# Kernel tuning notes

Hardware: AMD Instinct MI355X
Metric: run time of the kernel (lower is better)

## Reference

```python
import jax, jax.numpy as jnp
import numpy as np


def _gcn_norm(edge_index, n_nodes):
    # add self-loops, compute symmetric normalization coeffs (PyG gcn_norm)
    loop = jnp.arange(n_nodes, dtype=edge_index.dtype)
    src = jnp.concatenate([edge_index[0], loop])
    dst = jnp.concatenate([edge_index[1], loop])
    ones = jnp.ones(src.shape[0], dtype=jnp.float32)
    deg = jax.ops.segment_sum(ones, dst, num_segments=n_nodes)
    dinv = jnp.where(deg > 0, jax.lax.rsqrt(deg), 0.0)
    norm = dinv[src] * dinv[dst]  # (E + n_nodes,)
    return src, dst, norm


def _gcn_conv(x, W, b, src, dst, norm, n_nodes):
    h = x @ W                                   # (N, C_out) small dense GEMM first (PyG order)
    msg = h[src] * norm[:, None]                # gather + normalize
    out = jax.ops.segment_sum(msg, dst, num_segments=n_nodes)  # scatter-add aggregate
    return out + b


def setup_inputs() -> dict:
    key = jax.random.key(0)
    k1, k2, k3, k4, k5, k6 = jax.random.split(key, 6)
    n_nodes, n_edges = 100000, 1600000
    in_c, hid_c, out_c = 4, 32, 16
    x = jax.random.normal(k1, (n_nodes, in_c), dtype=jnp.float32)
    edge_index = jax.random.randint(k2, (2, n_edges), 0, n_nodes, dtype=jnp.int64)
    # Glorot init like PyG GCNConv.lin, zero bias
    s1 = float(np.sqrt(6.0 / (in_c + hid_c)))
    s2 = float(np.sqrt(6.0 / (hid_c + out_c)))
    W1 = jax.random.uniform(k3, (in_c, hid_c), jnp.float32, -s1, s1)
    b1 = jnp.zeros((hid_c,), jnp.float32)
    W2 = jax.random.uniform(k4, (hid_c, out_c), jnp.float32, -s2, s2)
    b2 = jnp.zeros((out_c,), jnp.float32)
    return {"x": x, "edge_index": edge_index, "W1": W1, "b1": b1, "W2": W2, "b2": b2}


def reference(x, edge_index, W1, b1, W2, b2):
    n_nodes = x.shape[0]
    src, dst, norm = _gcn_norm(edge_index, n_nodes)
    h = _gcn_conv(x, W1, b1, src, dst, norm, n_nodes)
    h = jax.nn.relu(h)
    # dropout is identity in eval mode
    z = _gcn_conv(h, W2, b2, src, dst, norm, n_nodes)
    return z
```

## Files before the change

kernel.cpp:

```cpp
#include <hip/hip_runtime.h>

constexpr int HID = 32;
constexpr int OUTC = 16;
constexpr int BIN = 256;
constexpr int BSH = 8;
constexpr int MAXNB = 1024;
constexpr int PSC = 512;
constexpr int PTILE = 2048;
constexpr int CAPC = 48;

typedef int iv4 __attribute__((ext_vector_type(4)));
typedef _Float16 h4 __attribute__((ext_vector_type(4)));

static __device__ __forceinline__ float4 ld4(const float* p) { return *(const float4*)p; }

__global__ void k_zero(int* __restrict__ bcnt) {
    bcnt[threadIdx.x] = 0;
}

__global__ void __launch_bounds__(256) k_part(
        const int* __restrict__ src, const int* __restrict__ dst,
        int* __restrict__ bcnt, int* __restrict__ elist,
        int E, int nb, int capb) {
    __shared__ int hist[PSC];
    __shared__ int lofs[PSC];
    __shared__ int gb[PSC];
    __shared__ int stage_e[PTILE];
    __shared__ short stage_b[PTILE];
    const int t = threadIdx.x;
    for (int i = t; i < PSC; i += 256) hist[i] = 0;
    __syncthreads();

    const int E4 = E >> 2;
    const int vbase = blockIdx.x * (PTILE / 4);
    int d[8], s[8], bn[8], r[8];
    bool val[2];
#pragma unroll
    for (int q = 0; q < 2; ++q) {
        const int v = vbase + q * 256 + t;
        val[q] = (v < E4);
        if (val[q]) {
            iv4 d4 = __builtin_nontemporal_load(((const iv4*)dst) + v);
            iv4 s4 = __builtin_nontemporal_load(((const iv4*)src) + v);
            d[q*4+0] = d4.x; d[q*4+1] = d4.y; d[q*4+2] = d4.z; d[q*4+3] = d4.w;
            s[q*4+0] = s4.x; s[q*4+1] = s4.y; s[q*4+2] = s4.z; s[q*4+3] = s4.w;
#pragma unroll
            for (int k = q*4; k < q*4+4; ++k) {
                bn[k] = d[k] >> BSH;
                r[k] = atomicAdd(&hist[bn[k]], 1);
            }
        }
    }
    __syncthreads();

    for (int i = t; i < PSC; i += 256) lofs[i] = hist[i];
    __syncthreads();
    int* cur = lofs; int* nxt = gb;
    for (int off = 1; off < PSC; off <<= 1) {
        for (int i = t; i < PSC; i += 256) nxt[i] = cur[i] + ((i >= off) ? cur[i - off] : 0);
        __syncthreads();
        int* tmp = cur; cur = nxt; nxt = tmp;
    }
    for (int i = t; i < PSC; i += 256) lofs[i] = cur[i] - hist[i];
    __syncthreads();
    for (int i = t; i < nb; i += 256) {
        int h = hist[i];
        gb[i] = h ? atomicAdd(&bcnt[i], h) : 0;
    }
#pragma unroll
    for (int q = 0; q < 2; ++q) {
        if (val[q]) {
#pragma unroll
            for (int k = q*4; k < q*4+4; ++k) {
                int pos = lofs[bn[k]] + r[k];
                stage_e[pos] = (s[k] << BSH) | (d[k] & (BIN-1));
                stage_b[pos] = (short)bn[k];
            }
        }
    }
    __syncthreads();

    const int handled = 4 * min(PSC, max(0, E4 - vbase));
    for (int i = t; i < handled; i += 256) {
        int b = stage_b[i];
        int p = gb[b] + (i - lofs[b]);
        if (p < capb) elist[(size_t)b * capb + p] = stage_e[i];
    }
    if (blockIdx.x == 0 && t < (E & 3)) {
        int j = (E4 << 2) + t;
        int dd = dst[j], ss = src[j];
        int bin = dd >> BSH;
        int pos = atomicAdd(&bcnt[bin], 1);
        if (pos < capb) elist[(size_t)bin * capb + pos] = (ss << BSH) | (dd & (BIN-1));
    }
}

__global__ void k_fill3(const int* __restrict__ elist, const int* __restrict__ bcnt,
                        int* __restrict__ cursor, int* __restrict__ eidx,
                        const float* __restrict__ x, float* __restrict__ dinv,
                        float* __restrict__ y, int capb, int N) {
    __shared__ int cnt[BIN];
    const int b = blockIdx.x;
    const int bin0 = b << BSH;
    const int tid = threadIdx.x;
    if (tid < BIN) cnt[tid] = 0;
    __syncthreads();
    const int ecnt = min(bcnt[b], capb);
    const int* lst = elist + (size_t)b * capb;
    for (int i0 = tid * 4; i0 + 3 < ecnt; i0 += blockDim.x * 4) {
        iv4 e = *(const iv4*)(lst + i0);
        int l0 = e.x & (BIN-1), s0 = (unsigned)e.x >> BSH;
        int l1 = e.y & (BIN-1), s1 = (unsigned)e.y >> BSH;
        int l2 = e.z & (BIN-1), s2 = (unsigned)e.z >> BSH;
        int l3 = e.w & (BIN-1), s3 = (unsigned)e.w >> BSH;
        int p0 = atomicAdd(&cnt[l0], 1);
        int p1 = atomicAdd(&cnt[l1], 1);
        int p2 = atomicAdd(&cnt[l2], 1);
        int p3 = atomicAdd(&cnt[l3], 1);
        if (p0 < CAPC) eidx[(size_t)(bin0 + l0) * CAPC + p0] = s0;
        if (p1 < CAPC) eidx[(size_t)(bin0 + l1) * CAPC + p1] = s1;
        if (p2 < CAPC) eidx[(size_t)(bin0 + l2) * CAPC + p2] = s2;
        if (p3 < CAPC) eidx[(size_t)(bin0 + l3) * CAPC + p3] = s3;
    }
    const int tb = ecnt & ~3;
    if (tid < (ecnt & 3)) {
        int e = lst[tb + tid];
        int l = e & (BIN-1);
        int pos = atomicAdd(&cnt[l], 1);
        if (pos < CAPC) eidx[(size_t)(bin0 + l) * CAPC + pos] = (unsigned)e >> BSH;
    }
    __syncthreads();
    const int node = bin0 + tid;
    if (tid < BIN && node < N) {
        int deg = cnt[tid];
        cursor[node] = deg;
        float di = 1.0f / sqrtf((float)(deg + 1));
        dinv[node] = di;
        float4 xv = ld4(x + (size_t)node * 4);
        float4 yv; yv.x = xv.x * di; yv.y = xv.y * di; yv.z = xv.z * di; yv.w = xv.w * di;
        *(float4*)(y + (size_t)node * 4) = yv;
    }
}

__global__ void __launch_bounds__(256) k_layer1(
        const int* __restrict__ eidx, const int* __restrict__ degv,
        const float* __restrict__ dinv, const float* __restrict__ y,
        const float* __restrict__ W1, const float* __restrict__ b1,
        const float* __restrict__ W2, _Float16* __restrict__ z, int N) {
    __shared__ float sW1[4 * HID];
    __shared__ float sb1[HID];
    __shared__ float sW2[HID * OUTC];
    __shared__ float4 sv_lds[64];
    const int tid = threadIdx.x;
    if (tid < 4 * HID) sW1[tid] = W1[tid];
    if (tid < HID) sb1[tid] = b1[tid];
    for (int i = tid; i < HID * OUTC; i += blockDim.x) sW2[i] = W2[i];
    __syncthreads();

    const int g = tid & 3;
    const int nl = tid >> 2;
    const int n = blockIdx.x * 64 + nl;
    if (n < N) {
        const int deg = min(degv[n], CAPC);
        const int* bucket = eidx + (size_t)n * CAPC;
        float4 a = {0,0,0,0};
        for (int base = g * 4; base + 3 < deg; base += 16) {
            iv4 q = *(const iv4*)(bucket + base);
            float4 y0 = ld4(y + (size_t)q.x * 4);
            float4 y1 = ld4(y + (size_t)q.y * 4);
            float4 y2 = ld4(y + (size_t)q.z * 4);
            float4 y3 = ld4(y + (size_t)q.w * 4);
            a.x += (y0.x + y1.x) + (y2.x + y3.x);
            a.y += (y0.y + y1.y) + (y2.y + y3.y);
            a.z += (y0.z + y1.z) + (y2.z + y3.z);
            a.w += (y0.w + y1.w) + (y2.w + y3.w);
        }
        const int tb = deg & ~3;
        if (g < (deg & 3)) {
            float4 yv = ld4(y + (size_t)bucket[tb + g] * 4);
            a.x += yv.x; a.y += yv.y; a.z += yv.z; a.w += yv.w;
        }
        a.x += __shfl_xor(a.x, 1); a.y += __shfl_xor(a.y, 1);
        a.z += __shfl_xor(a.z, 1); a.w += __shfl_xor(a.w, 1);
        a.x += __shfl_xor(a.x, 2); a.y += __shfl_xor(a.y, 2);
        a.z += __shfl_xor(a.z, 2); a.w += __shfl_xor(a.w, 2);
        if (g == 0) sv_lds[nl] = a;
    }
    __syncthreads();

    if (tid < 64) {
        const int n2 = blockIdx.x * 64 + tid;
        if (n2 < N) {
            const float di = dinv[n2];
            float4 a = sv_lds[tid];
            float4 yn = ld4(y + (size_t)n2 * 4);
            float4 sv;
            sv.x = (a.x + yn.x) * di;
            sv.y = (a.y + yn.y) * di;
            sv.z = (a.z + yn.z) * di;
            sv.w = (a.w + yn.w) * di;
            float r[HID];
#pragma unroll
            for (int c = 0; c < HID; ++c)
                r[c] = fmaxf(sv.x * sW1[c] + sv.y * sW1[HID + c] +
                             sv.z * sW1[2*HID + c] + sv.w * sW1[3*HID + c] + sb1[c], 0.f);
            float o[OUTC] = {};
#pragma unroll
            for (int k = 0; k < HID; ++k) {
                const float rk = r[k];
#pragma unroll
                for (int c = 0; c < OUTC; ++c) o[c] += rk * sW2[k * OUTC + c];
            }
            _Float16* op = z + (size_t)n2 * OUTC;
#pragma unroll
            for (int c = 0; c < OUTC; c += 4) {
                h4 v;
                v.x = (_Float16)(o[c+0] * di);
                v.y = (_Float16)(o[c+1] * di);
                v.z = (_Float16)(o[c+2] * di);
                v.w = (_Float16)(o[c+3] * di);
                *(h4*)(op + c) = v;
            }
        }
    }
}

__global__ void __launch_bounds__(256) k_agg2(
        const int* __restrict__ eidx, const int* __restrict__ degv,
        const float* __restrict__ dinv, const _Float16* __restrict__ z,
        const float* __restrict__ b2, float* __restrict__ out, int N) {
    __shared__ float sb[OUTC];
    if (threadIdx.x < OUTC) sb[threadIdx.x] = b2[threadIdx.x];
    __syncthreads();
    const int tid = threadIdx.x;
    const int l4 = (tid & 3) * 4;
    const int n = blockIdx.x * (blockDim.x >> 2) + (tid >> 2);
    if (n >= N) return;
    const int deg = min(degv[n], CAPC);
    const int* bucket = eidx + (size_t)n * CAPC;
    float4 a0 = {0,0,0,0}, a1 = {0,0,0,0}, a2 = {0,0,0,0}, a3 = {0,0,0,0};
    int i = 0;
    for (; i + 15 < deg; i += 16) {
        iv4 q0 = *(const iv4*)(bucket + i);
        iv4 q1 = *(const iv4*)(bucket + i + 4);
        iv4 q2 = *(const iv4*)(bucket + i + 8);
        iv4 q3 = *(const iv4*)(bucket + i + 12);
        h4 r0 = *(const h4*)(z + (size_t)q0.x * OUTC + l4);
        h4 r1 = *(const h4*)(z + (size_t)q0.y * OUTC + l4);
        h4 r2 = *(const h4*)(z + (size_t)q0.z * OUTC + l4);
        h4 r3 = *(const h4*)(z + (size_t)q0.w * OUTC + l4);
        h4 r4 = *(const h4*)(z + (size_t)q1.x * OUTC + l4);
        h4 r5 = *(const h4*)(z + (size_t)q1.y * OUTC + l4);
        h4 r6 = *(const h4*)(z + (size_t)q1.z * OUTC + l4);
        h4 r7 = *(const h4*)(z + (size_t)q1.w * OUTC + l4);
        h4 r8 = *(const h4*)(z + (size_t)q2.x * OUTC + l4);
        h4 r9 = *(const h4*)(z + (size_t)q2.y * OUTC + l4);
        h4 ra = *(const h4*)(z + (size_t)q2.z * OUTC + l4);
        h4 rb = *(const h4*)(z + (size_t)q2.w * OUTC + l4);
        h4 rc = *(const h4*)(z + (size_t)q3.x * OUTC + l4);
        h4 rd = *(const h4*)(z + (size_t)q3.y * OUTC + l4);
        h4 re = *(const h4*)(z + (size_t)q3.z * OUTC + l4);
        h4 rf = *(const h4*)(z + (size_t)q3.w * OUTC + l4);
        a0.x += (float)r0.x + (float)r1.x; a0.y += (float)r0.y + (float)r1.y;
        a0.z += (float)r0.z + (float)r1.z; a0.w += (float)r0.w + (float)r1.w;
        a1.x += (float)r2.x + (float)r3.x; a1.y += (float)r2.y + (float)r3.y;
        a1.z += (float)r2.z + (float)r3.z; a1.w += (float)r2.w + (float)r3.w;
        a2.x += (float)r4.x + (float)r5.x; a2.y += (float)r4.y + (float)r5.y;
        a2.z += (float)r4.z + (float)r5.z; a2.w += (float)r4.w + (float)r5.w;
        a3.x += (float)r6.x + (float)r7.x; a3.y += (float)r6.y + (float)r7.y;
        a3.z += (float)r6.z + (float)r7.z; a3.w += (float)r6.w + (float)r7.w;
        a0.x += (float)r8.x + (float)r9.x; a0.y += (float)r8.y + (float)r9.y;
        a0.z += (float)r8.z + (float)r9.z; a0.w += (float)r8.w + (float)r9.w;
        a1.x += (float)ra.x + (float)rb.x; a1.y += (float)ra.y + (float)rb.y;
        a1.z += (float)ra.z + (float)rb.z; a1.w += (float)ra.w + (float)rb.w;
        a2.x += (float)rc.x + (float)rd.x; a2.y += (float)rc.y + (float)rd.y;
        a2.z += (float)rc.z + (float)rd.z; a2.w += (float)rc.w + (float)rd.w;
        a3.x += (float)re.x + (float)rf.x; a3.y += (float)re.y + (float)rf.y;
        a3.z += (float)re.z + (float)rf.z; a3.w += (float)re.w + (float)rf.w;
    }
    for (; i + 3 < deg; i += 4) {
        iv4 q0 = *(const iv4*)(bucket + i);
        h4 r0 = *(const h4*)(z + (size_t)q0.x * OUTC + l4);
        h4 r1 = *(const h4*)(z + (size_t)q0.y * OUTC + l4);
        h4 r2 = *(const h4*)(z + (size_t)q0.z * OUTC + l4);
        h4 r3 = *(const h4*)(z + (size_t)q0.w * OUTC + l4);
        a0.x += (float)r0.x + (float)r1.x; a0.y += (float)r0.y + (float)r1.y;
        a0.z += (float)r0.z + (float)r1.z; a0.w += (float)r0.w + (float)r1.w;
        a1.x += (float)r2.x + (float)r3.x; a1.y += (float)r2.y + (float)r3.y;
        a1.z += (float)r2.z + (float)r3.z; a1.w += (float)r2.w + (float)r3.w;
    }
    for (; i < deg; ++i) {
        h4 r = *(const h4*)(z + (size_t)bucket[i] * OUTC + l4);
        a0.x += (float)r.x; a0.y += (float)r.y; a0.z += (float)r.z; a0.w += (float)r.w;
    }
    const float di = dinv[n];
    h4 zn = *(const h4*)(z + (size_t)n * OUTC + l4);
    float4 o;
    o.x = ((a0.x + a1.x) + (a2.x + a3.x) + (float)zn.x) * di + sb[l4 + 0];
    o.y = ((a0.y + a1.y) + (a2.y + a3.y) + (float)zn.y) * di + sb[l4 + 1];
    o.z = ((a0.z + a1.z) + (a2.z + a3.z) + (float)zn.z) * di + sb[l4 + 2];
    o.w = ((a0.w + a1.w) + (a2.w + a3.w) + (float)zn.w) * di + sb[l4 + 3];
    *(float4*)(out + (size_t)n * OUTC + l4) = o;
}

extern "C" void kernel_launch(void* const* d_in, const int* in_sizes, int n_in,
                              void* d_out, int out_size, void* d_ws, size_t ws_size,
                              hipStream_t stream) {
    const float* x  = (const float*)d_in[0];
    const int*   ei = (const int*)d_in[1];
    const float* W1 = (const float*)d_in[2];
    const float* b1 = (const float*)d_in[3];
    const float* W2 = (const float*)d_in[4];
    const float* b2 = (const float*)d_in[5];

    const int N = in_sizes[0] / 4;
    const int E = in_sizes[1] / 2;
    const int* src = ei;
    const int* dst = ei + E;

    const int nb = (N + BIN - 1) >> BSH;

    auto align = [](size_t v) { return (v + 255) & ~(size_t)255; };
    int capb = (E / nb + 1024 + 3) & ~3;
    {
        size_t fixed = align((size_t)N * 4) + align((size_t)MAXNB * 4) +
                       align((size_t)N * 4) + align((size_t)N * 4 * 4) +
                       align((size_t)N * OUTC * 2) + align((size_t)N * CAPC * 4);
        while (capb > E / nb + 128 && fixed + align((size_t)nb * (size_t)capb * 4) > ws_size)
            capb -= 256;
    }

    char* ws = (char*)d_ws;
    size_t off = 0;
    int*      cursor = (int*)(ws + off);      off += align((size_t)N * 4);
    int*      bcnt   = (int*)(ws + off);      off += align((size_t)MAXNB * 4);
    float*    dinv   = (float*)(ws + off);    off += align((size_t)N * 4);
    float*    y      = (float*)(ws + off);    off += align((size_t)N * 4 * 4);
    _Float16* z      = (_Float16*)(ws + off); off += align((size_t)N * OUTC * 2);
    int*      eidx   = (int*)(ws + off);      off += align((size_t)N * CAPC * 4);
    int*      elist  = (int*)(ws + off);      off += align((size_t)nb * (size_t)capb * 4);
    (void)n_in;

    k_zero<<<1, MAXNB, 0, stream>>>(bcnt);
    k_part<<<(E + PTILE - 1) / PTILE, 256, 0, stream>>>(src, dst, bcnt, elist, E, nb, capb);
    k_fill3<<<nb, 512, 0, stream>>>(elist, bcnt, cursor, eidx, x, dinv, y, capb, N);
    k_layer1<<<(N + 63) / 64, 256, 0, stream>>>(eidx, cursor, dinv, y, W1, b1, W2, z, N);
    k_agg2<<<(N + 63) / 64, 256, 0, stream>>>(eidx, cursor, dinv, z, b2, (float*)d_out, N);
    (void)out_size;
}
```

Measured before the change: 85.73 us.

## Fuse all GCN stages into one persistent cooperative kernel with grid syncs

Replaces the five separate launches (zero, partition, fill, layer1, agg2) with one cooperative persistent kernel. Blocks loop over the work items of each stage, and grid.sync() separates the stages. Shared memory is a union sized for the largest stage. The goal is to remove per-launch overhead and the idle gaps between kernels; the cost is grid-wide barriers and occupancy capped by the partition stage's shared-memory footprint. The fill stage also moves from 512 to 256 threads per block. If the cooperative launch fails, the code falls back to separate launches.

```diff
diff --git a/kernel.cpp b/kernel.cpp
--- a/kernel.cpp
+++ b/kernel.cpp
@@ -1,4 +1,7 @@
 #include <hip/hip_runtime.h>
+#include <hip/hip_cooperative_groups.h>
+
+namespace cg = cooperative_groups;
 
 constexpr int HID = 32;
 constexpr int OUTC = 16;
@@ -14,25 +17,32 @@
 
 static __device__ __forceinline__ float4 ld4(const float* p) { return *(const float4*)p; }
 
-__global__ void k_zero(int* __restrict__ bcnt) {
-    bcnt[threadIdx.x] = 0;
-}
-
-__global__ void __launch_bounds__(256) k_part(
-        const int* __restrict__ src, const int* __restrict__ dst,
-        int* __restrict__ bcnt, int* __restrict__ elist,
-        int E, int nb, int capb) {
-    __shared__ int hist[PSC];
-    __shared__ int lofs[PSC];
-    __shared__ int gb[PSC];
-    __shared__ int stage_e[PTILE];
-    __shared__ short stage_b[PTILE];
+struct Params {
+    const int* src; const int* dst;
+    const float* x; const float* W1; const float* b1;
+    const float* W2; const float* b2;
+    float* out;
+    int* cursor; int* bcnt; float* dinv; float* y;
+    _Float16* z; int* eidx; int* elist;
+    int E, N, nb, capb, nchunks, ngroups;
+};
+
+struct SmemPart {
+    int hist[PSC]; int lofs[PSC]; int gb[PSC];
+    int stage_e[PTILE]; short stage_b[PTILE];
+};
+struct SmemL1 { float sW1[4*HID]; float sb1[HID]; float sW2[HID*OUTC]; float4 sv[64]; };
+struct SmemF3 { int cnt[BIN]; };
+struct SmemA2 { float sb[OUTC]; };
+
+
+static __device__ void part_chunk(const Params& p, char* smem, int c) {
+    SmemPart* S = (SmemPart*)smem;
     const int t = threadIdx.x;
-    for (int i = t; i < PSC; i += 256) hist[i] = 0;
-    __syncthreads();
-
-    const int E4 = E >> 2;
-    const int vbase = blockIdx.x * (PTILE / 4);
+    for (int i = t; i < PSC; i += 256) S->hist[i] = 0;
+    __syncthreads();
+    const int E4 = p.E >> 2;
+    const int vbase = c * (PTILE / 4);
     int d[8], s[8], bn[8], r[8];
     bool val[2];
 #pragma unroll
@@ -40,136 +50,129 @@
         const int v = vbase + q * 256 + t;
         val[q] = (v < E4);
         if (val[q]) {
-            iv4 d4 = __builtin_nontemporal_load(((const iv4*)dst) + v);
-            iv4 s4 = __builtin_nontemporal_load(((const iv4*)src) + v);
+            iv4 d4 = __builtin_nontemporal_load(((const iv4*)p.dst) + v);
+            iv4 s4 = __builtin_nontemporal_load(((const iv4*)p.src) + v);
             d[q*4+0] = d4.x; d[q*4+1] = d4.y; d[q*4+2] = d4.z; d[q*4+3] = d4.w;
             s[q*4+0] = s4.x; s[q*4+1] = s4.y; s[q*4+2] = s4.z; s[q*4+3] = s4.w;
 #pragma unroll
             for (int k = q*4; k < q*4+4; ++k) {
                 bn[k] = d[k] >> BSH;
-                r[k] = atomicAdd(&hist[bn[k]], 1);
+                r[k] = atomicAdd(&S->hist[bn[k]], 1);
             }
         }
     }
     __syncthreads();
-
-    for (int i = t; i < PSC; i += 256) lofs[i] = hist[i];
-    __syncthreads();
-    int* cur = lofs; int* nxt = gb;
+    for (int i = t; i < PSC; i += 256) S->lofs[i] = S->hist[i];
+    __syncthreads();
+    int* cur = S->lofs; int* nxt = S->gb;
     for (int off = 1; off < PSC; off <<= 1) {
         for (int i = t; i < PSC; i += 256) nxt[i] = cur[i] + ((i >= off) ? cur[i - off] : 0);
         __syncthreads();
         int* tmp = cur; cur = nxt; nxt = tmp;
     }
-    for (int i = t; i < PSC; i += 256) lofs[i] = cur[i] - hist[i];
-    __syncthreads();
-    for (int i = t; i < nb; i += 256) {
-        int h = hist[i];
-        gb[i] = h ? atomicAdd(&bcnt[i], h) : 0;
+    for (int i = t; i < PSC; i += 256) S->lofs[i] = cur[i] - S->hist[i];
+    __syncthreads();
+    for (int i = t; i < p.nb; i += 256) {
+        int h = S->hist[i];
+        S->gb[i] = h ? atomicAdd(&p.bcnt[i], h) : 0;
     }
 #pragma unroll
     for (int q = 0; q < 2; ++q) {
         if (val[q]) {
 #pragma unroll
             for (int k = q*4; k < q*4+4; ++k) {
-                int pos = lofs[bn[k]] + r[k];
-                stage_e[pos] = (s[k] << BSH) | (d[k] & (BIN-1));
-                stage_b[pos] = (short)bn[k];
+                int pos = S->lofs[bn[k]] + r[k];
+                S->stage_e[pos] = (s[k] << BSH) | (d[k] & (BIN-1));
+                S->stage_b[pos] = (short)bn[k];
             }
         }
     }
     __syncthreads();
-
     const int handled = 4 * min(PSC, max(0, E4 - vbase));
     for (int i = t; i < handled; i += 256) {
-        int b = stage_b[i];
-        int p = gb[b] + (i - lofs[b]);
-        if (p < capb) elist[(size_t)b * capb + p] = stage_e[i];
-    }
-    if (blockIdx.x == 0 && t < (E & 3)) {
-        int j = (E4 << 2) + t;
-        int dd = dst[j], ss = src[j];
+        int b = S->stage_b[i];
+        int pp = S->gb[b] + (i - S->lofs[b]);
+        if (pp < p.capb) p.elist[(size_t)b * p.capb + pp] = S->stage_e[i];
+    }
+}
+
+static __device__ void part_tail(const Params& p) {
+    if (threadIdx.x < (p.E & 3)) {
+        int j = (p.E & ~3) + threadIdx.x;
+        int dd = p.dst[j], ss = p.src[j];
         int bin = dd >> BSH;
-        int pos = atomicAdd(&bcnt[bin], 1);
-        if (pos < capb) elist[(size_t)bin * capb + pos] = (ss << BSH) | (dd & (BIN-1));
-    }
-}
-
-__global__ void k_fill3(const int* __restrict__ elist, const int* __restrict__ bcnt,
-                        int* __restrict__ cursor, int* __restrict__ eidx,
-                        const float* __restrict__ x, float* __restrict__ dinv,
-                        float* __restrict__ y, int capb, int N) {
-    __shared__ int cnt[BIN];
-    const int b = blockIdx.x;
+        int pos = atomicAdd(&p.bcnt[bin], 1);
+        if (pos < p.capb) p.elist[(size_t)bin * p.capb + pos] = (ss << BSH) | (dd & (BIN-1));
+    }
+}
+
+static __device__ void fill3_bin(const Params& p, char* smem, int b) {
+    SmemF3* S = (SmemF3*)smem;
     const int bin0 = b << BSH;
     const int tid = threadIdx.x;
-    if (tid < BIN) cnt[tid] = 0;
-    __syncthreads();
-    const int ecnt = min(bcnt[b], capb);
-    const int* lst = elist + (size_t)b * capb;
-    for (int i0 = tid * 4; i0 + 3 < ecnt; i0 += blockDim.x * 4) {
+    if (tid < BIN) S->cnt[tid] = 0;
+    __syncthreads();
+    const int ecnt = min(p.bcnt[b], p.capb);
+    const int* lst = p.elist + (size_t)b * p.capb;
+    for (int i0 = tid * 4; i0 + 3 < ecnt; i0 += 256 * 4) {
         iv4 e = *(const iv4*)(lst + i0);
         int l0 = e.x & (BIN-1), s0 = (unsigned)e.x >> BSH;
         int l1 = e.y & (BIN-1), s1 = (unsigned)e.y >> BSH;
         int l2 = e.z & (BIN-1), s2 = (unsigned)e.z >> BSH;
         int l3 = e.w & (BIN-1), s3 = (unsigned)e.w >> BSH;
-        int p0 = atomicAdd(&cnt[l0], 1);
-        int p1 = atomicAdd(&cnt[l1], 1);
-        int p2 = atomicAdd(&cnt[l2], 1);
-        int p3 = atomicAdd(&cnt[l3], 1);
-        if (p0 < CAPC) eidx[(size_t)(bin0 + l0) * CAPC + p0] = s0;
-        if (p1 < CAPC) eidx[(size_t)(bin0 + l1) * CAPC + p1] = s1;
-        if (p2 < CAPC) eidx[(size_t)(bin0 + l2) * CAPC + p2] = s2;
-        if (p3 < CAPC) eidx[(size_t)(bin0 + l3) * CAPC + p3] = s3;
+        int p0 = atomicAdd(&S->cnt[l0], 1);
+        int p1 = atomicAdd(&S->cnt[l1], 1);
+        int p2 = atomicAdd(&S->cnt[l2], 1);
+        int p3 = atomicAdd(&S->cnt[l3], 1);
+        if (p0 < CAPC) p.eidx[(size_t)(bin0 + l0) * CAPC + p0] = s0;
+        if (p1 < CAPC) p.eidx[(size_t)(bin0 + l1) * CAPC + p1] = s1;
+        if (p2 < CAPC) p.eidx[(size_t)(bin0 + l2) * CAPC + p2] = s2;
+        if (p3 < CAPC) p.eidx[(size_t)(bin0 + l3) * CAPC + p3] = s3;
     }
     const int tb = ecnt & ~3;
     if (tid < (ecnt & 3)) {
         int e = lst[tb + tid];
         int l = e & (BIN-1);
-        int pos = atomicAdd(&cnt[l], 1);
-        if (pos < CAPC) eidx[(size_t)(bin0 + l) * CAPC + pos] = (unsigned)e >> BSH;
+        int pos = atomicAdd(&S->cnt[l], 1);
+        if (pos < CAPC) p.eidx[(size_t)(bin0 + l) * CAPC + pos] = (unsigned)e >> BSH;
     }
     __syncthreads();
     const int node = bin0 + tid;
-    if (tid < BIN && node < N) {
-        int deg = cnt[tid];
-        cursor[node] = deg;
+    if (tid < BIN && node < p.N) {
+        int deg = S->cnt[tid];
+        p.cursor[node] = deg;
         float di = 1.0f / sqrtf((float)(deg + 1));
-        dinv[node] = di;
-        float4 xv = ld4(x + (size_t)node * 4);
-        float4 yv; yv.x = xv.x * di; yv.y = xv.y * di; yv.z = xv.z * di; yv.w = xv.w * di;
-        *(float4*)(y + (size_t)node * 4) = yv;
-    }
-}
-
-__global__ void __launch_bounds__(256) k_layer1(
-        const int* __restrict__ eidx, const int* __restrict__ degv,
-        const float* __restrict__ dinv, const float* __restrict__ y,
-        const float* __restrict__ W1, const float* __restrict__ b1,
-        const float* __restrict__ W2, _Float16* __restrict__ z, int N) {
-    __shared__ float sW1[4 * HID];
-    __shared__ float sb1[HID];
-    __shared__ float sW2[HID * OUTC];
-    __shared__ float4 sv_lds[64];
+        p.dinv[node] = di;
+        float4 xv = ld4(p.x + (size_t)node * 4);
+        float4 yv; yv.x = xv.x*di; yv.y = xv.y*di; yv.z = xv.z*di; yv.w = xv.w*di;
+        *(float4*)(p.y + (size_t)node * 4) = yv;
+    }
+}
+
+static __device__ void layer1_weights(const Params& p, char* smem) {
+    SmemL1* S = (SmemL1*)smem;
     const int tid = threadIdx.x;
-    if (tid < 4 * HID) sW1[tid] = W1[tid];
-    if (tid < HID) sb1[tid] = b1[tid];
-    for (int i = tid; i < HID * OUTC; i += blockDim.x) sW2[i] = W2[i];
-    __syncthreads();
-
+    if (tid < 4 * HID) S->sW1[tid] = p.W1[tid];
+    if (tid < HID) S->sb1[tid] = p.b1[tid];
+    for (int i = tid; i < HID * OUTC; i += 256) S->sW2[i] = p.W2[i];
+}
+
+static __device__ void layer1_group(const Params& p, char* smem, int grp) {
+    SmemL1* S = (SmemL1*)smem;
+    const int tid = threadIdx.x;
     const int g = tid & 3;
     const int nl = tid >> 2;
-    const int n = blockIdx.x * 64 + nl;
-    if (n < N) {
-        const int deg = min(degv[n], CAPC);
-        const int* bucket = eidx + (size_t)n * CAPC;
+    const int n = grp * 64 + nl;
+    if (n < p.N) {
+        const int deg = min(p.cursor[n], CAPC);
+        const int* bucket = p.eidx + (size_t)n * CAPC;
         float4 a = {0,0,0,0};
         for (int base = g * 4; base + 3 < deg; base += 16) {
             iv4 q = *(const iv4*)(bucket + base);
-            float4 y0 = ld4(y + (size_t)q.x * 4);
-            float4 y1 = ld4(y + (size_t)q.y * 4);
-            float4 y2 = ld4(y + (size_t)q.z * 4);
-            float4 y3 = ld4(y + (size_t)q.w * 4);
+            float4 y0 = ld4(p.y + (size_t)q.x * 4);
+            float4 y1 = ld4(p.y + (size_t)q.y * 4);
+            float4 y2 = ld4(p.y + (size_t)q.z * 4);
+            float4 y3 = ld4(p.y + (size_t)q.w * 4);
             a.x += (y0.x + y1.x) + (y2.x + y3.x);
             a.y += (y0.y + y1.y) + (y2.y + y3.y);
             a.z += (y0.z + y1.z) + (y2.z + y3.z);
@@ -177,67 +180,57 @@
         }
         const int tb = deg & ~3;
         if (g < (deg & 3)) {
-            float4 yv = ld4(y + (size_t)bucket[tb + g] * 4);
+            float4 yv = ld4(p.y + (size_t)bucket[tb + g] * 4);
             a.x += yv.x; a.y += yv.y; a.z += yv.z; a.w += yv.w;
         }
         a.x += __shfl_xor(a.x, 1); a.y += __shfl_xor(a.y, 1);
         a.z += __shfl_xor(a.z, 1); a.w += __shfl_xor(a.w, 1);
         a.x += __shfl_xor(a.x, 2); a.y += __shfl_xor(a.y, 2);
         a.z += __shfl_xor(a.z, 2); a.w += __shfl_xor(a.w, 2);
-        if (g == 0) sv_lds[nl] = a;
-    }
-    __syncthreads();
-
+        if (g == 0) S->sv[nl] = a;
+    }
+    __syncthreads();
     if (tid < 64) {
-        const int n2 = blockIdx.x * 64 + tid;
-        if (n2 < N) {
-            const float di = dinv[n2];
-            float4 a = sv_lds[tid];
-            float4 yn = ld4(y + (size_t)n2 * 4);
+        const int n2 = grp * 64 + tid;
+        if (n2 < p.N) {
+            const float di = p.dinv[n2];
+            float4 a = S->sv[tid];
+            float4 yn = ld4(p.y + (size_t)n2 * 4);
             float4 sv;
-            sv.x = (a.x + yn.x) * di;
-            sv.y = (a.y + yn.y) * di;
-            sv.z = (a.z + yn.z) * di;
-            sv.w = (a.w + yn.w) * di;
+            sv.x = (a.x + yn.x) * di; sv.y = (a.y + yn.y) * di;
+            sv.z = (a.z + yn.z) * di; sv.w = (a.w + yn.w) * di;
             float r[HID];
 #pragma unroll
             for (int c = 0; c < HID; ++c)
-                r[c] = fmaxf(sv.x * sW1[c] + sv.y * sW1[HID + c] +
-                             sv.z * sW1[2*HID + c] + sv.w * sW1[3*HID + c] + sb1[c], 0.f);
+                r[c] = fmaxf(sv.x * S->sW1[c] + sv.y * S->sW1[HID + c] +
+                             sv.z * S->sW1[2*HID + c] + sv.w * S->sW1[3*HID + c] + S->sb1[c], 0.f);
             float o[OUTC] = {};
 #pragma unroll
             for (int k = 0; k < HID; ++k) {
                 const float rk = r[k];
 #pragma unroll
-                for (int c = 0; c < OUTC; ++c) o[c] += rk * sW2[k * OUTC + c];
+                for (int c = 0; c < OUTC; ++c) o[c] += rk * S->sW2[k * OUTC + c];
             }
-            _Float16* op = z + (size_t)n2 * OUTC;
+            _Float16* op = p.z + (size_t)n2 * OUTC;
 #pragma unroll
             for (int c = 0; c < OUTC; c += 4) {
                 h4 v;
-                v.x = (_Float16)(o[c+0] * di);
-                v.y = (_Float16)(o[c+1] * di);
-                v.z = (_Float16)(o[c+2] * di);
-                v.w = (_Float16)(o[c+3] * di);
+                v.x = (_Float16)(o[c+0] * di); v.y = (_Float16)(o[c+1] * di);
+                v.z = (_Float16)(o[c+2] * di); v.w = (_Float16)(o[c+3] * di);
                 *(h4*)(op + c) = v;
             }
         }
     }
 }
 
-__global__ void __launch_bounds__(256) k_agg2(
-        const int* __restrict__ eidx, const int* __restrict__ degv,
-        const float* __restrict__ dinv, const _Float16* __restrict__ z,
-        const float* __restrict__ b2, float* __restrict__ out, int N) {
-    __shared__ float sb[OUTC];
-    if (threadIdx.x < OUTC) sb[threadIdx.x] = b2[threadIdx.x];
-    __syncthreads();
+static __device__ void agg2_group(const Params& p, const float* sb, int grp) {
     const int tid = threadIdx.x;
     const int l4 = (tid & 3) * 4;
-    const int n = blockIdx.x * (blockDim.x >> 2) + (tid >> 2);
-    if (n >= N) return;
-    const int deg = min(degv[n], CAPC);
-    const int* bucket = eidx + (size_t)n * CAPC;
+    const int n = grp * 64 + (tid >> 2);
+    if (n >= p.N) return;
+    const int deg = min(p.cursor[n], CAPC);
+    const int* bucket = p.eidx + (size_t)n * CAPC;
+    const _Float16* z = p.z;
     float4 a0 = {0,0,0,0}, a1 = {0,0,0,0}, a2 = {0,0,0,0}, a3 = {0,0,0,0};
     int i = 0;
     for (; i + 15 < deg; i += 16) {
@@ -293,58 +286,145 @@
         h4 r = *(const h4*)(z + (size_t)bucket[i] * OUTC + l4);
         a0.x += (float)r.x; a0.y += (float)r.y; a0.z += (float)r.z; a0.w += (float)r.w;
     }
-    const float di = dinv[n];
+    const float di = p.dinv[n];
     h4 zn = *(const h4*)(z + (size_t)n * OUTC + l4);
     float4 o;
     o.x = ((a0.x + a1.x) + (a2.x + a3.x) + (float)zn.x) * di + sb[l4 + 0];
     o.y = ((a0.y + a1.y) + (a2.y + a3.y) + (float)zn.y) * di + sb[l4 + 1];
     o.z = ((a0.z + a1.z) + (a2.z + a3.z) + (float)zn.z) * di + sb[l4 + 2];
     o.w = ((a0.w + a1.w) + (a2.w + a3.w) + (float)zn.w) * di + sb[l4 + 3];
-    *(float4*)(out + (size_t)n * OUTC + l4) = o;
+    *(float4*)(p.out + (size_t)n * OUTC + l4) = o;
+}
+
+
+__global__ void __launch_bounds__(256) k_mega(Params p) {
+    __shared__ __align__(16) char smem[sizeof(SmemPart)];
+    cg::grid_group grid = cg::this_grid();
+    const int gid = blockIdx.x;
+
+    for (int i = gid * 256 + threadIdx.x; i < MAXNB; i += gridDim.x * 256) p.bcnt[i] = 0;
+    grid.sync();
+
+    for (int c = gid; c < p.nchunks; c += gridDim.x) {
+        __syncthreads();
+        part_chunk(p, smem, c);
+    }
+    if (gid == 0) part_tail(p);
+    grid.sync();
+
+    for (int b = gid; b < p.nb; b += gridDim.x) {
+        __syncthreads();
+        fill3_bin(p, smem, b);
+    }
+    grid.sync();
+
+    layer1_weights(p, smem);
+    for (int grp = gid; grp < p.ngroups; grp += gridDim.x) {
+        __syncthreads();
+        layer1_group(p, smem, grp);
+    }
+    grid.sync();
+
+    {
+        SmemA2* S = (SmemA2*)smem;
+        __syncthreads();
+        if (threadIdx.x < OUTC) S->sb[threadIdx.x] = p.b2[threadIdx.x];
+        __syncthreads();
+        for (int grp = gid; grp < p.ngroups; grp += gridDim.x)
+            agg2_group(p, S->sb, grp);
+    }
+}
+
+
+__global__ void k_zero(int* __restrict__ bcnt) { bcnt[threadIdx.x] = 0; }
+
+__global__ void __launch_bounds__(256) k_part_f(Params p) {
+    __shared__ __align__(16) char smem[sizeof(SmemPart)];
+    part_chunk(p, smem, blockIdx.x);
+    if (blockIdx.x == 0) part_tail(p);
+}
+
+__global__ void __launch_bounds__(256) k_fill3_f(Params p) {
+    __shared__ __align__(16) char smem[sizeof(SmemF3)];
+    fill3_bin(p, smem, blockIdx.x);
+}
+
+__global__ void __launch_bounds__(256) k_layer1_f(Params p) {
+    __shared__ __align__(16) char smem[sizeof(SmemL1)];
+    layer1_weights(p, smem);
+    __syncthreads();
+    layer1_group(p, smem, blockIdx.x);
+}
+
+__global__ void __launch_bounds__(256) k_agg2_f(Params p) {
+    __shared__ float sb[OUTC];
+    if (threadIdx.x < OUTC) sb[threadIdx.x] = p.b2[threadIdx.x];
+    __syncthreads();
+    agg2_group(p, sb, blockIdx.x);
 }
 
 extern "C" void kernel_launch(void* const* d_in, const int* in_sizes, int n_in,
                               void* d_out, int out_size, void* d_ws, size_t ws_size,
                               hipStream_t stream) {
-    const float* x  = (const float*)d_in[0];
-    const int*   ei = (const int*)d_in[1];
-    const float* W1 = (const float*)d_in[2];
-    const float* b1 = (const float*)d_in[3];
-    const float* W2 = (const float*)d_in[4];
-    const float* b2 = (const float*)d_in[5];
-
-    const int N = in_sizes[0] / 4;
-    const int E = in_sizes[1] / 2;
-    const int* src = ei;
-    const int* dst = ei + E;
-
-    const int nb = (N + BIN - 1) >> BSH;
+    Params p;
+    p.x  = (const float*)d_in[0];
+    const int* ei = (const int*)d_in[1];
+    p.W1 = (const float*)d_in[2];
+    p.b1 = (const float*)d_in[3];
+    p.W2 = (const float*)d_in[4];
+    p.b2 = (const float*)d_in[5];
+    p.out = (float*)d_out;
+
+    p.N = in_sizes[0] / 4;
+    p.E = in_sizes[1] / 2;
+    p.src = ei;
+    p.dst = ei + p.E;
+    p.nb = (p.N + BIN - 1) >> BSH;
+    p.nchunks = ((p.E >> 2) + (PTILE/4) - 1) / (PTILE/4);
+    p.ngroups = (p.N + 63) / 64;
 
     auto align = [](size_t v) { return (v + 255) & ~(size_t)255; };
-    int capb = (E / nb + 1024 + 3) & ~3;
+    int capb = (p.E / p.nb + 1024 + 3) & ~3;
     {
-        size_t fixed = align((size_t)N * 4) + align((size_t)MAXNB * 4) +
-                       align((size_t)N * 4) + align((size_t)N * 4 * 4) +
-                       align((size_t)N * OUTC * 2) + align((size_t)N * CAPC * 4);
-        while (capb > E / nb + 128 && fixed + align((size_t)nb * (size_t)capb * 4) > ws_size)
+        size_t fixed = align((size_t)p.N * 4) + align((size_t)MAXNB * 4) +
+                       align((size_t)p.N * 4) + align((size_t)p.N * 4 * 4) +
+                       align((size_t)p.N * OUTC * 2) + align((size_t)p.N * CAPC * 4);
+        while (capb > p.E / p.nb + 128 &&
+               fixed + align((size_t)p.nb * (size_t)capb * 4) > ws_size)
             capb -= 256;
     }
+    p.capb = capb;
 
     char* ws = (char*)d_ws;
     size_t off = 0;
-    int*      cursor = (int*)(ws + off);      off += align((size_t)N * 4);
-    int*      bcnt   = (int*)(ws + off);      off += align((size_t)MAXNB * 4);
-    float*    dinv   = (float*)(ws + off);    off += align((size_t)N * 4);
-    float*    y      = (float*)(ws + off);    off += align((size_t)N * 4 * 4);
-    _Float16* z      = (_Float16*)(ws + off); off += align((size_t)N * OUTC * 2);
-    int*      eidx   = (int*)(ws + off);      off += align((size_t)N * CAPC * 4);
-    int*      elist  = (int*)(ws + off);      off += align((size_t)nb * (size_t)capb * 4);
-    (void)n_in;
-
-    k_zero<<<1, MAXNB, 0, stream>>>(bcnt);
-    k_part<<<(E + PTILE - 1) / PTILE, 256, 0, stream>>>(src, dst, bcnt, elist, E, nb, capb);
-    k_fill3<<<nb, 512, 0, stream>>>(elist, bcnt, cursor, eidx, x, dinv, y, capb, N);
-    k_layer1<<<(N + 63) / 64, 256, 0, stream>>>(eidx, cursor, dinv, y, W1, b1, W2, z, N);
-    k_agg2<<<(N + 63) / 64, 256, 0, stream>>>(eidx, cursor, dinv, z, b2, (float*)d_out, N);
-    (void)out_size;
-}
+    p.cursor = (int*)(ws + off);      off += align((size_t)p.N * 4);
+    p.bcnt   = (int*)(ws + off);      off += align((size_t)MAXNB * 4);
+    p.dinv   = (float*)(ws + off);    off += align((size_t)p.N * 4);
+    p.y      = (float*)(ws + off);    off += align((size_t)p.N * 4 * 4);
+    p.z      = (_Float16*)(ws + off); off += align((size_t)p.N * OUTC * 2);
+    p.eidx   = (int*)(ws + off);      off += align((size_t)p.N * CAPC * 4);
+    p.elist  = (int*)(ws + off);      off += align((size_t)p.nb * (size_t)capb * 4);
+    (void)n_in; (void)out_size;
+
+    int dev = 0;
+    (void)hipGetDevice(&dev);
+    int nCU = 256;
+    (void)hipDeviceGetAttribute(&nCU, hipDeviceAttributeMultiprocessorCount, dev);
+    int maxB = 0;
+    hipError_t oe = hipOccupancyMaxActiveBlocksPerMultiprocessor(&maxB, k_mega, 256, 0);
+    if (oe != hipSuccess || maxB < 1) maxB = 2;
+    int grid = maxB * nCU;
+    if (grid > p.ngroups) grid = p.ngroups;
+    if (grid < 1) grid = 1;
+
+    void* args[] = { &p };
+    hipError_t le = hipLaunchCooperativeKernel((void*)k_mega, dim3(grid), dim3(256),
+                                               args, 0, stream);
+    if (le == hipSuccess) return;
+
+    k_zero<<<1, MAXNB, 0, stream>>>(p.bcnt);
+    k_part_f<<<p.nchunks, 256, 0, stream>>>(p);
+    k_fill3_f<<<p.nb, 256, 0, stream>>>(p);
+    k_layer1_f<<<p.ngroups, 256, 0, stream>>>(p);
+    k_agg2_f<<<p.ngroups, 256, 0, stream>>>(p);
+}
```

New measurement: 334.9 us. +290.6%, slower.
